# Kernel optimization log

Hardware: AMD Instinct MI355X
Metric: run time of the kernel (lower is better)

## Reference

```python
import jax, jax.numpy as jnp
import numpy as np

N_IN = 250000
N_OUT = 500000
INC = 256
OUTC = 128
KVOL = 8  # 2x2x2 transposed-conv kernel volume
BN_EPS = 1e-5


def setup_inputs() -> dict:
    key = jax.random.key(0)
    k1, k2, k3 = jax.random.split(key, 3)
    x = jax.random.normal(k1, (N_IN, INC), dtype=jnp.float32)
    # sparse conv weight: one [inc, outc] matrix per kernel offset
    W = jax.random.normal(k2, (KVOL, INC, OUTC), dtype=jnp.float32) * 0.02
    gamma = jnp.ones((OUTC,), dtype=jnp.float32)
    beta = jnp.zeros((OUTC,), dtype=jnp.float32)
    # kernel map: destination output voxel for each (kernel offset, input voxel)
    out_idx = jax.random.randint(k3, (KVOL, N_IN), 0, N_OUT, dtype=jnp.int32)
    return {"x": x, "W": W, "gamma": gamma, "beta": beta,
            "out_idx": out_idx, "n_out": N_OUT}


def reference(x, W, gamma, beta, out_idx, n_out):
    # --- sparse transposed conv3d: gather-matmul-scatter per kernel offset ---
    out = jnp.zeros((n_out, W.shape[-1]), dtype=x.dtype)
    for k in range(W.shape[0]):  # fixed small kernel volume (8)
        out = out.at[out_idx[k]].add(x @ W[k])
    # --- BatchNorm (training-mode batch stats over all output voxels) ---
    mean = jnp.mean(out, axis=0)
    var = jnp.mean(jnp.square(out - mean), axis=0)
    y = (out - mean) * jax.lax.rsqrt(var + BN_EPS) * gamma + beta
    return y
```

## Files before the change

### kernel.cpp

```cpp
#include <hip/hip_runtime.h>
#include <hip/hip_bf16.h>
#include <stdint.h>

#define N_IN 250000
#define N_OUT 500000
#define INC 256
#define OUTC 128
#define KVOL 8
#define NTOT (KVOL * N_IN)
#define BN_EPS 1e-5f

typedef __bf16 bf16x8_t __attribute__((ext_vector_type(8)));
typedef __bf16 bf16x4_t __attribute__((ext_vector_type(4)));
typedef float f32x4_t __attribute__((ext_vector_type(4)));

__device__ __forceinline__ __bf16 f2bf(float x) {
  union { float f; uint32_t u; } v; v.f = x;
  uint32_t r = v.u + 0x7FFFu + ((v.u >> 16) & 1u);
  uint16_t h = (uint16_t)(r >> 16);
  union { uint16_t s; __bf16 b; } o; o.s = h;
  return o.b;
}

__device__ __forceinline__ uint32_t pack2bf(float lo, float hi) {
  union { float f; uint32_t u; } a, b; a.f = lo; b.f = hi;
  uint32_t ra = a.u + 0x7FFFu + ((a.u >> 16) & 1u);
  uint32_t rb = b.u + 0x7FFFu + ((b.u >> 16) & 1u);
  return (ra >> 16) | (rb & 0xFFFF0000u);
}

__device__ __forceinline__ float bflo(uint32_t w) {
  union { uint32_t u; float f; } v; v.u = w << 16; return v.f;
}
__device__ __forceinline__ float bfhi(uint32_t w) {
  union { uint32_t u; float f; } v; v.u = w & 0xFFFF0000u; return v.f;
}

__global__ void wconv_kernel(const float* __restrict__ W, __bf16* __restrict__ Wt) {
  int f = blockIdx.x * blockDim.x + threadIdx.x;
  if (f >= KVOL * OUTC * INC) return;
  int i = f & (INC - 1);
  int o = (f >> 8) & (OUTC - 1);
  int k = f >> 15;
  Wt[f] = f2bf(W[(k * INC + i) * OUTC + o]);
}


__global__ void hist_kernel(const int* __restrict__ oidx, int* __restrict__ cnt) {
  int g = blockIdx.x * 256 + threadIdx.x;
  if (g < NTOT) atomicAdd(&cnt[oidx[g]], 1);
}

__global__ void scan1_kernel(const int* __restrict__ cnt, int* __restrict__ offs,
                             int* __restrict__ bsum) {
  __shared__ int sd[256];
  int t = threadIdx.x;
  int base = blockIdx.x * 1024 + t * 4;
  int v0 = 0, v1 = 0, v2 = 0, v3 = 0;
  if (base + 3 < N_OUT) {
    int4 v = *(const int4*)&cnt[base];
    v0 = v.x; v1 = v.y; v2 = v.z; v3 = v.w;
  } else {
    if (base     < N_OUT) v0 = cnt[base];
    if (base + 1 < N_OUT) v1 = cnt[base + 1];
    if (base + 2 < N_OUT) v2 = cnt[base + 2];
  }
  int s = v0 + v1 + v2 + v3;
  sd[t] = s; __syncthreads();
  for (int o = 1; o < 256; o <<= 1) {
    int a = (t >= o) ? sd[t - o] : 0;
    __syncthreads();
    sd[t] += a;
    __syncthreads();
  }
  int excl = sd[t] - s;
  if (base     < N_OUT) offs[base]     = excl;
  if (base + 1 < N_OUT) offs[base + 1] = excl + v0;
  if (base + 2 < N_OUT) offs[base + 2] = excl + v0 + v1;
  if (base + 3 < N_OUT) offs[base + 3] = excl + v0 + v1 + v2;
  if (t == 255) bsum[blockIdx.x] = sd[255];
}

__global__ void scan2_kernel(const int* __restrict__ bsum, int* __restrict__ bsumx, int nb) {
  __shared__ int sd[512];
  int t = threadIdx.x;
  int s = (t < nb) ? bsum[t] : 0;
  sd[t] = s; __syncthreads();
  for (int o = 1; o < 512; o <<= 1) {
    int a = (t >= o) ? sd[t - o] : 0;
    __syncthreads();
    sd[t] += a;
    __syncthreads();
  }
  if (t < nb) bsumx[t] = sd[t] - s;
}

__global__ void scan3_kernel(int* __restrict__ offs, int* __restrict__ cursor,
                             const int* __restrict__ bsumx) {
  int g = blockIdx.x * 256 + threadIdx.x;
  if (g < N_OUT) {
    int v = offs[g] + bsumx[g >> 10];
    offs[g] = v;
    cursor[g] = v;
  }
  if (g == 0) offs[N_OUT] = NTOT;
}

__global__ void fill_kernel(const int* __restrict__ oidx, int* __restrict__ cursor,
                            int* __restrict__ slot) {
  int g = blockIdx.x * 256 + threadIdx.x;
  if (g < NTOT) {
    int d = oidx[g];
    slot[g] = atomicAdd(&cursor[d], 1);
  }
}


#define TM 64
#define LDS_STRIDE 264

__global__ __launch_bounds__(512, 1) void gemm_store_kernel(
    const float* __restrict__ x, const __bf16* __restrict__ Wt,
    const int* __restrict__ slot, char* __restrict__ partials) {
  __shared__ __bf16 xs[TM * LDS_STRIDE];
  __shared__ uint2 stg[8][16][34];
  const int t = threadIdx.x;
  const int row0 = blockIdx.x * TM;

  #pragma unroll
  for (int i = 0; i < 8; ++i) {
    int f = t + i * 512;
    int r = f >> 6;
    int c4 = f & 63;
    int grow = row0 + r;
    float4 v = make_float4(0.f, 0.f, 0.f, 0.f);
    if (grow < N_IN) v = ((const float4*)x)[(size_t)grow * 64 + c4];
    bf16x4_t bv;
    bv[0] = f2bf(v.x); bv[1] = f2bf(v.y); bv[2] = f2bf(v.z); bv[3] = f2bf(v.w);
    *(bf16x4_t*)&xs[r * LDS_STRIDE + c4 * 4] = bv;
  }
  __syncthreads();

  const int w  = t >> 6;
  const int l  = t & 63;
  const int lr = l & 15;
  const int lg = l >> 4;

  f32x4_t accT[8][4];
  #pragma unroll
  for (int n = 0; n < 8; ++n)
    #pragma unroll
    for (int m = 0; m < 4; ++m)
      accT[n][m] = (f32x4_t){0.f, 0.f, 0.f, 0.f};

  const __bf16* Wk = Wt + (size_t)w * OUTC * INC;

  #pragma unroll
  for (int s = 0; s < 8; ++s) {
    bf16x8_t a[4], b[8];
    #pragma unroll
    for (int m = 0; m < 4; ++m)
      a[m] = *(const bf16x8_t*)&xs[(m * 16 + lr) * LDS_STRIDE + s * 32 + lg * 8];
    #pragma unroll
    for (int n = 0; n < 8; ++n)
      b[n] = *(const bf16x8_t*)&Wk[(n * 16 + lr) * INC + s * 32 + lg * 8];
    #pragma unroll
    for (int n = 0; n < 8; ++n)
      #pragma unroll
      for (int m = 0; m < 4; ++m)
        accT[n][m] = __builtin_amdgcn_mfma_f32_16x16x32_bf16(b[n], a[m], accT[n][m], 0, 0, 0);
  }

  const int r = l >> 2;
  const int p = l & 3;
  #pragma unroll
  for (int m = 0; m < 4; ++m) {
    #pragma unroll
    for (int n = 0; n < 8; ++n) {
      uint2 pk;
      pk.x = pack2bf(accT[n][m][0], accT[n][m][1]);
      pk.y = pack2bf(accT[n][m][2], accT[n][m][3]);
      stg[w][lr][n * 4 + lg] = pk;
    }
    __syncthreads();
    int grow = row0 + 16 * m + r;
    if (grow < N_IN) {
      int sl = slot[w * N_IN + grow];
      const uint4* rp = (const uint4*)&stg[w][r][0];
      char* dst = partials + (size_t)sl * 256 + p * 64;
      #pragma unroll
      for (int q = 0; q < 4; ++q)
        *(uint4*)(dst + q * 16) = rp[p * 4 + q];
    }
    __syncthreads();
  }
}


__global__ __launch_bounds__(256) void reduce_stats_kernel(
    const char* __restrict__ partials, const int* __restrict__ offs,
    char* __restrict__ accb, float* __restrict__ stats) {
  const int t = threadIdx.x;
  const int lane16 = t & 15;
  const int grp = t >> 4;
  float s[8], q[8];
  #pragma unroll
  for (int i = 0; i < 8; ++i) { s[i] = 0.f; q[i] = 0.f; }

  for (int d = blockIdx.x * 16 + grp; d < N_OUT; d += gridDim.x * 16) {
    int j0 = offs[d], j1 = offs[d + 1];
    float a[8];
    #pragma unroll
    for (int i = 0; i < 8; ++i) a[i] = 0.f;
    for (int j = j0; j < j1; ++j) {
      uint4 v = *(const uint4*)(partials + (size_t)j * 256 + lane16 * 16);
      a[0] += bflo(v.x); a[1] += bfhi(v.x);
      a[2] += bflo(v.y); a[3] += bfhi(v.y);
      a[4] += bflo(v.z); a[5] += bfhi(v.z);
      a[6] += bflo(v.w); a[7] += bfhi(v.w);
    }
    uint4 o;
    o.x = pack2bf(a[0], a[1]); o.y = pack2bf(a[2], a[3]);
    o.z = pack2bf(a[4], a[5]); o.w = pack2bf(a[6], a[7]);
    *(uint4*)(accb + (size_t)d * 512 + lane16 * 16) = o;
    uint32_t wd[4] = {o.x, o.y, o.z, o.w};
    #pragma unroll
    for (int u = 0; u < 4; ++u) {
      float f0 = bflo(wd[u]), f1 = bfhi(wd[u]);
      s[2 * u] += f0;     q[2 * u] += f0 * f0;
      s[2 * u + 1] += f1; q[2 * u + 1] += f1 * f1;
    }
  }

  __shared__ float reds[16][16][8];
  __shared__ float redq[16][16][8];
  #pragma unroll
  for (int i = 0; i < 8; ++i) { reds[grp][lane16][i] = s[i]; redq[grp][lane16][i] = q[i]; }
  __syncthreads();
  if (t < 128) {
    float acc = 0.f;
    #pragma unroll
    for (int g2 = 0; g2 < 16; ++g2) acc += reds[g2][t >> 3][t & 7];
    atomicAdd(&stats[t], acc);
  } else {
    int c = t - 128;
    float acc = 0.f;
    #pragma unroll
    for (int g2 = 0; g2 < 16; ++g2) acc += redq[g2][c >> 3][c & 7];
    atomicAdd(&stats[128 + c], acc);
  }
}

__global__ void norm_kernel(char* __restrict__ outb, const float* __restrict__ stats,
                            const float* __restrict__ gamma, const float* __restrict__ beta) {
  const int t = threadIdx.x;
  const int j = t & 15;
  const int ro = t >> 4;
  const float inv_n = 1.0f / (float)N_OUT;
  float sc[8], sh[8];
  #pragma unroll
  for (int i = 0; i < 8; ++i) {
    int c = j * 8 + i;
    float mean = stats[c] * inv_n;
    float var  = stats[128 + c] * inv_n - mean * mean;
    float s = gamma[c] * rsqrtf(var + BN_EPS);
    sc[i] = s;
    sh[i] = beta[c] - mean * s;
  }
  for (int r = blockIdx.x * 16 + ro; r < N_OUT; r += gridDim.x * 16) {
    uint4 v = *(const uint4*)(outb + (size_t)r * 512 + j * 16);
    uint32_t wds[4] = {v.x, v.y, v.z, v.w};
    f32x4_t o0, o1;
    #pragma unroll
    for (int u = 0; u < 4; ++u) {
      float f0 = bflo(wds[u]) * sc[2 * u] + sh[2 * u];
      float f1 = bfhi(wds[u]) * sc[2 * u + 1] + sh[2 * u + 1];
      if (u < 2) { o0[2 * u] = f0; o0[2 * u + 1] = f1; }
      else       { o1[2 * (u - 2)] = f0; o1[2 * (u - 2) + 1] = f1; }
    }
    *(f32x4_t*)(outb + (size_t)r * 512 + j * 32) = o0;
    *(f32x4_t*)(outb + (size_t)r * 512 + j * 32 + 16) = o1;
  }
}


__global__ __launch_bounds__(512, 1) void gemm_scatter_f32_kernel(
    const float* __restrict__ x, const __bf16* __restrict__ Wt,
    const int* __restrict__ out_idx, float* __restrict__ acc) {
  __shared__ __bf16 xs[TM * LDS_STRIDE];
  const int t = threadIdx.x;
  const int row0 = blockIdx.x * TM;
  #pragma unroll
  for (int i = 0; i < 8; ++i) {
    int f = t + i * 512;
    int r = f >> 6;
    int c4 = f & 63;
    int grow = row0 + r;
    float4 v = make_float4(0.f, 0.f, 0.f, 0.f);
    if (grow < N_IN) v = ((const float4*)x)[(size_t)grow * 64 + c4];
    bf16x4_t bv;
    bv[0] = f2bf(v.x); bv[1] = f2bf(v.y); bv[2] = f2bf(v.z); bv[3] = f2bf(v.w);
    *(bf16x4_t*)&xs[r * LDS_STRIDE + c4 * 4] = bv;
  }
  __syncthreads();
  const int w = t >> 6, l = t & 63, lr = l & 15, lg = l >> 4;
  f32x4_t accr[4][8];
  #pragma unroll
  for (int m = 0; m < 4; ++m)
    #pragma unroll
    for (int n = 0; n < 8; ++n)
      accr[m][n] = (f32x4_t){0.f, 0.f, 0.f, 0.f};
  const __bf16* Wk = Wt + (size_t)w * OUTC * INC;
  #pragma unroll
  for (int s = 0; s < 8; ++s) {
    bf16x8_t a[4], b[8];
    #pragma unroll
    for (int m = 0; m < 4; ++m)
      a[m] = *(const bf16x8_t*)&xs[(m * 16 + lr) * LDS_STRIDE + s * 32 + lg * 8];
    #pragma unroll
    for (int n = 0; n < 8; ++n)
      b[n] = *(const bf16x8_t*)&Wk[(n * 16 + lr) * INC + s * 32 + lg * 8];
    #pragma unroll
    for (int m = 0; m < 4; ++m)
      #pragma unroll
      for (int n = 0; n < 8; ++n)
        accr[m][n] = __builtin_amdgcn_mfma_f32_16x16x32_bf16(a[m], b[n], accr[m][n], 0, 0, 0);
  }
  const int* oidx = out_idx + (size_t)w * N_IN;
  #pragma unroll
  for (int m = 0; m < 4; ++m) {
    int rbase = m * 16 + lg * 4;
    #pragma unroll
    for (int reg = 0; reg < 4; ++reg) {
      int grow = row0 + rbase + reg;
      if (grow < N_IN) {
        int dst = oidx[grow];
        float* ap = acc + (size_t)dst * OUTC;
        #pragma unroll
        for (int n = 0; n < 8; ++n)
          atomicAdd(&ap[n * 16 + lr], accr[m][n][reg]);
      }
    }
  }
}

__global__ void stats_f32_kernel(const float* __restrict__ acc, float* __restrict__ stats) {
  const int t = threadIdx.x;
  const int c4 = t & 31;
  const int ro = t >> 5;
  f32x4_t s = {0.f, 0.f, 0.f, 0.f}, q = {0.f, 0.f, 0.f, 0.f};
  for (int r = blockIdx.x * 8 + ro; r < N_OUT; r += gridDim.x * 8) {
    f32x4_t v = ((const f32x4_t*)acc)[(size_t)r * 32 + c4];
    s += v; q += v * v;
  }
  __shared__ float red[256][8];
  #pragma unroll
  for (int j = 0; j < 4; ++j) { red[t][j] = s[j]; red[t][4 + j] = q[j]; }
  __syncthreads();
  if (t < 32) {
    float S[4] = {0.f, 0.f, 0.f, 0.f}, Q[4] = {0.f, 0.f, 0.f, 0.f};
    for (int r2 = 0; r2 < 8; ++r2)
      #pragma unroll
      for (int j = 0; j < 4; ++j) {
        S[j] += red[r2 * 32 + t][j];
        Q[j] += red[r2 * 32 + t][4 + j];
      }
    #pragma unroll
    for (int j = 0; j < 4; ++j) {
      atomicAdd(&stats[t * 4 + j], S[j]);
      atomicAdd(&stats[128 + t * 4 + j], Q[j]);
    }
  }
}

__global__ void norm_f32_kernel(float* __restrict__ out, const float* __restrict__ stats,
                                const float* __restrict__ gamma, const float* __restrict__ beta) {
  const int t = threadIdx.x;
  const int c4 = t & 31;
  const int ro = t >> 5;
  const float inv_n = 1.0f / (float)N_OUT;
  float sc[4], sh[4];
  #pragma unroll
  for (int j = 0; j < 4; ++j) {
    int c = c4 * 4 + j;
    float mean = stats[c] * inv_n;
    float var  = stats[128 + c] * inv_n - mean * mean;
    float s = gamma[c] * rsqrtf(var + BN_EPS);
    sc[j] = s;
    sh[j] = beta[c] - mean * s;
  }
  for (int r = blockIdx.x * 8 + ro; r < N_OUT; r += gridDim.x * 8) {
    f32x4_t v = ((const f32x4_t*)out)[(size_t)r * 32 + c4];
    #pragma unroll
    for (int j = 0; j < 4; ++j) v[j] = v[j] * sc[j] + sh[j];
    ((f32x4_t*)out)[(size_t)r * 32 + c4] = v;
  }
}


extern "C" void kernel_launch(void* const* d_in, const int* in_sizes, int n_in,
                              void* d_out, int out_size, void* d_ws, size_t ws_size,
                              hipStream_t stream) {
  const float* x     = (const float*)d_in[0];
  const float* W     = (const float*)d_in[1];
  const float* gamma = (const float*)d_in[2];
  const float* beta  = (const float*)d_in[3];
  const int*   oidx  = (const int*)d_in[4];

  const size_t P_OFF     = 0;
  const size_t SLOT_OFF  = 512000000;
  const size_t CNT_OFF   = 520000000;
  const size_t OFFS_OFF  = 522000000;
  const size_t CURS_OFF  = 524000384;
  const size_t BSUM_OFF  = 526000384;
  const size_t BSUMX_OFF = 526004480;
  const size_t WT_OFF    = 526008576;
  const size_t STATS_OFF = 526532864;
  const size_t NEED      = 526533888;

  if (ws_size >= NEED) {
    char* ws = (char*)d_ws;
    char* partials = ws + P_OFF;
    int* slot   = (int*)(ws + SLOT_OFF);
    int* cnt    = (int*)(ws + CNT_OFF);
    int* offs   = (int*)(ws + OFFS_OFF);
    int* cursor = (int*)(ws + CURS_OFF);
    int* bsum   = (int*)(ws + BSUM_OFF);
    int* bsumx  = (int*)(ws + BSUMX_OFF);
    __bf16* Wt  = (__bf16*)(ws + WT_OFF);
    float* stats = (float*)(ws + STATS_OFF);

    hipMemsetAsync(cnt, 0, N_OUT * sizeof(int), stream);
    hipMemsetAsync(stats, 0, 256 * sizeof(float), stream);

    wconv_kernel<<<(KVOL * OUTC * INC + 255) / 256, 256, 0, stream>>>(W, Wt);
    hist_kernel<<<(NTOT + 255) / 256, 256, 0, stream>>>(oidx, cnt);
    const int NB1 = (N_OUT + 1023) / 1024;
    scan1_kernel<<<NB1, 256, 0, stream>>>(cnt, offs, bsum);
    scan2_kernel<<<1, 512, 0, stream>>>(bsum, bsumx, NB1);
    scan3_kernel<<<(N_OUT + 255) / 256, 256, 0, stream>>>(offs, cursor, bsumx);
    fill_kernel<<<(NTOT + 255) / 256, 256, 0, stream>>>(oidx, cursor, slot);
    gemm_store_kernel<<<(N_IN + TM - 1) / TM, 512, 0, stream>>>(x, Wt, slot, partials);
    reduce_stats_kernel<<<2048, 256, 0, stream>>>(partials, offs, (char*)d_out, stats);
    norm_kernel<<<512, 256, 0, stream>>>((char*)d_out, stats, gamma, beta);
  } else {
    __bf16* Wt   = (__bf16*)d_ws;
    float* stats = (float*)((char*)d_ws + (size_t)KVOL * OUTC * INC * 2);
    float* out = (float*)d_out;

    hipMemsetAsync(d_out, 0, (size_t)N_OUT * OUTC * sizeof(float), stream);
    hipMemsetAsync(stats, 0, 256 * sizeof(float), stream);

    wconv_kernel<<<(KVOL * OUTC * INC + 255) / 256, 256, 0, stream>>>(W, Wt);
    gemm_scatter_f32_kernel<<<(N_IN + TM - 1) / TM, 512, 0, stream>>>(x, Wt, oidx, out);
    stats_f32_kernel<<<1024, 256, 0, stream>>>(out, stats);
    norm_f32_kernel<<<2048, 256, 0, stream>>>(out, stats, gamma, beta);
  }
}
```

Baseline: 918.0 us.

## Sort inputs per kernel offset and gather rows so partial writes are localized

Builds per-offset destination-sorted orderings of input rows via extra histogram/scan/fill passes, pre-converts x to bf16 once, and launches the GEMM per (row tile, offset) gathering x rows in sorted order. The intent is to make partial-sum stores land in nearby slots instead of scattered ones, improving write locality. It adds extra atomics, scan kernels and gather reads, reduces per-block weight reuse, and uses the output buffer as scratch space.

```diff
diff --git a/kernel.cpp b/kernel.cpp
--- a/kernel.cpp
+++ b/kernel.cpp
@@ -9,6 +9,7 @@
 #define KVOL 8
 #define NTOT (KVOL * N_IN)
 #define BN_EPS 1e-5f
+#define DCHUNKS 489
 
 typedef __bf16 bf16x8_t __attribute__((ext_vector_type(8)));
 typedef __bf16 bf16x4_t __attribute__((ext_vector_type(4)));
@@ -17,8 +18,7 @@
 __device__ __forceinline__ __bf16 f2bf(float x) {
   union { float f; uint32_t u; } v; v.f = x;
   uint32_t r = v.u + 0x7FFFu + ((v.u >> 16) & 1u);
-  uint16_t h = (uint16_t)(r >> 16);
-  union { uint16_t s; __bf16 b; } o; o.s = h;
+  union { uint16_t s; __bf16 b; } o; o.s = (uint16_t)(r >> 16);
   return o.b;
 }
 
@@ -34,6 +34,18 @@
 }
 __device__ __forceinline__ float bfhi(uint32_t w) {
   union { uint32_t u; float f; } v; v.u = w & 0xFFFF0000u; return v.f;
+}
+
+
+__global__ void xconv_kernel(const float* __restrict__ x, uint32_t* __restrict__ xb) {
+  int g = blockIdx.x * 256 + threadIdx.x;
+  if (g >= N_IN * INC / 8) return;
+  const float4* p = (const float4*)x + (size_t)g * 2;
+  float4 v0 = p[0], v1 = p[1];
+  uint4 o;
+  o.x = pack2bf(v0.x, v0.y); o.y = pack2bf(v0.z, v0.w);
+  o.z = pack2bf(v1.x, v1.y); o.w = pack2bf(v1.z, v1.w);
+  ((uint4*)xb)[g] = o;
 }
 
 __global__ void wconv_kernel(const float* __restrict__ W, __bf16* __restrict__ Wt) {
@@ -46,87 +58,264 @@
 }
 
 
-__global__ void hist_kernel(const int* __restrict__ oidx, int* __restrict__ cnt) {
-  int g = blockIdx.x * 256 + threadIdx.x;
-  if (g < NTOT) atomicAdd(&cnt[oidx[g]], 1);
-}
-
-__global__ void scan1_kernel(const int* __restrict__ cnt, int* __restrict__ offs,
-                             int* __restrict__ bsum) {
+__global__ void hist8_kernel(const int* __restrict__ oidx, int* __restrict__ cnt8,
+                             int* __restrict__ gcnt) {
+  int i = blockIdx.x * 256 + threadIdx.x;
+  int k = blockIdx.y;
+  if (i < N_IN) {
+    int d = oidx[k * N_IN + i];
+    atomicAdd(&cnt8[k * N_OUT + d], 1);
+    atomicAdd(&gcnt[d], 1);
+  }
+}
+
+__global__ void scan1s_kernel(const int* __restrict__ in, int* __restrict__ out,
+                              int* __restrict__ bsum) {
   __shared__ int sd[256];
   int t = threadIdx.x;
+  int s = blockIdx.y;
+  const int* inp = in + (size_t)s * N_OUT;
+  int* outp = out + (size_t)s * N_OUT;
   int base = blockIdx.x * 1024 + t * 4;
   int v0 = 0, v1 = 0, v2 = 0, v3 = 0;
   if (base + 3 < N_OUT) {
-    int4 v = *(const int4*)&cnt[base];
+    int4 v = *(const int4*)&inp[base];
     v0 = v.x; v1 = v.y; v2 = v.z; v3 = v.w;
   } else {
-    if (base     < N_OUT) v0 = cnt[base];
-    if (base + 1 < N_OUT) v1 = cnt[base + 1];
-    if (base + 2 < N_OUT) v2 = cnt[base + 2];
-  }
-  int s = v0 + v1 + v2 + v3;
-  sd[t] = s; __syncthreads();
+    if (base     < N_OUT) v0 = inp[base];
+    if (base + 1 < N_OUT) v1 = inp[base + 1];
+    if (base + 2 < N_OUT) v2 = inp[base + 2];
+  }
+  int sm = v0 + v1 + v2 + v3;
+  sd[t] = sm; __syncthreads();
   for (int o = 1; o < 256; o <<= 1) {
     int a = (t >= o) ? sd[t - o] : 0;
     __syncthreads();
     sd[t] += a;
     __syncthreads();
   }
-  int excl = sd[t] - s;
-  if (base     < N_OUT) offs[base]     = excl;
-  if (base + 1 < N_OUT) offs[base + 1] = excl + v0;
-  if (base + 2 < N_OUT) offs[base + 2] = excl + v0 + v1;
-  if (base + 3 < N_OUT) offs[base + 3] = excl + v0 + v1 + v2;
-  if (t == 255) bsum[blockIdx.x] = sd[255];
-}
-
-__global__ void scan2_kernel(const int* __restrict__ bsum, int* __restrict__ bsumx, int nb) {
+  int excl = sd[t] - sm;
+  if (base     < N_OUT) outp[base]     = excl;
+  if (base + 1 < N_OUT) outp[base + 1] = excl + v0;
+  if (base + 2 < N_OUT) outp[base + 2] = excl + v0 + v1;
+  if (base + 3 < N_OUT) outp[base + 3] = excl + v0 + v1 + v2;
+  if (t == 255) bsum[s * DCHUNKS + blockIdx.x] = sd[255];
+}
+
+__global__ void scan2s_kernel(const int* __restrict__ bsum, int* __restrict__ bsumx) {
   __shared__ int sd[512];
   int t = threadIdx.x;
-  int s = (t < nb) ? bsum[t] : 0;
-  sd[t] = s; __syncthreads();
+  int s = blockIdx.x;
+  int v = (t < DCHUNKS) ? bsum[s * DCHUNKS + t] : 0;
+  sd[t] = v; __syncthreads();
   for (int o = 1; o < 512; o <<= 1) {
     int a = (t >= o) ? sd[t - o] : 0;
     __syncthreads();
     sd[t] += a;
     __syncthreads();
   }
-  if (t < nb) bsumx[t] = sd[t] - s;
-}
-
-__global__ void scan3_kernel(int* __restrict__ offs, int* __restrict__ cursor,
-                             const int* __restrict__ bsumx) {
+  if (t < DCHUNKS) bsumx[s * DCHUNKS + t] = sd[t] - v;
+}
+
+__global__ void scan3s_kernel(int* __restrict__ cur8, const int* __restrict__ bsumx) {
+  int g = blockIdx.x * 256 + threadIdx.x;
+  int s = blockIdx.y;
+  if (g < N_OUT) cur8[(size_t)s * N_OUT + g] += bsumx[s * DCHUNKS + (g >> 10)];
+}
+
+__global__ void scan3g_kernel(int* __restrict__ goffs, int* __restrict__ gcur,
+                              const int* __restrict__ bsumx) {
   int g = blockIdx.x * 256 + threadIdx.x;
   if (g < N_OUT) {
-    int v = offs[g] + bsumx[g >> 10];
-    offs[g] = v;
-    cursor[g] = v;
-  }
-  if (g == 0) offs[N_OUT] = NTOT;
-}
-
-__global__ void fill_kernel(const int* __restrict__ oidx, int* __restrict__ cursor,
-                            int* __restrict__ slot) {
-  int g = blockIdx.x * 256 + threadIdx.x;
-  if (g < NTOT) {
-    int d = oidx[g];
-    slot[g] = atomicAdd(&cursor[d], 1);
-  }
-}
-
-
-#define TM 64
+    int v = goffs[g] + bsumx[g >> 10];
+    goffs[g] = v;
+    gcur[g] = v;
+  }
+  if (g == 0) goffs[N_OUT] = NTOT;
+}
+
+__global__ void fill_kernel(const int* __restrict__ oidx, int* __restrict__ cur8,
+                            int* __restrict__ gcur, int* __restrict__ ssrc,
+                            int* __restrict__ sgslot) {
+  int i = blockIdx.x * 256 + threadIdx.x;
+  int k = blockIdx.y;
+  if (i < N_IN) {
+    int d = oidx[k * N_IN + i];
+    int j = atomicAdd(&cur8[(size_t)k * N_OUT + d], 1);
+    int g = atomicAdd(&gcur[d], 1);
+    ssrc[k * N_IN + j] = i;
+    sgslot[k * N_IN + j] = g;
+  }
+}
+
+
+#define GTM 64
 #define LDS_STRIDE 264
 
-__global__ __launch_bounds__(512, 1) void gemm_store_kernel(
+__global__ __launch_bounds__(512, 1) void gemm_gather_store_kernel(
+    const uint32_t* __restrict__ xb, const __bf16* __restrict__ Wt,
+    const int* __restrict__ ssrc, const int* __restrict__ sgslot,
+    char* __restrict__ partials) {
+  __shared__ __bf16 xs[GTM * LDS_STRIDE];
+  __shared__ uint2 stg[GTM][34];
+  __shared__ int s_src[GTM], s_gsl[GTM];
+  const int t = threadIdx.x;
+  const int k = blockIdx.y;
+  const int slot0 = blockIdx.x * GTM;
+
+  if (t < GTM) {
+    int sl = slot0 + t;
+    s_src[t] = (sl < N_IN) ? ssrc[k * N_IN + sl] : -1;
+    s_gsl[t] = (sl < N_IN) ? sgslot[k * N_IN + sl] : -1;
+  }
+  __syncthreads();
+
+  #pragma unroll
+  for (int ii = 0; ii < 4; ++ii) {
+    int r = ii * 16 + (t >> 5);
+    int off = t & 31;
+    int src = s_src[r];
+    uint4 v = {0u, 0u, 0u, 0u};
+    if (src >= 0) v = *(const uint4*)((const char*)xb + (size_t)src * 512 + off * 16);
+    *(uint4*)&xs[r * LDS_STRIDE + off * 8] = v;
+  }
+  __syncthreads();
+
+  const int w = t >> 6, l = t & 63, lr = l & 15, lg = l >> 4;
+  const int m  = w >> 1;
+  const int nh = w & 1;
+
+  f32x4_t accT[4];
+  #pragma unroll
+  for (int n = 0; n < 4; ++n) accT[n] = (f32x4_t){0.f, 0.f, 0.f, 0.f};
+
+  const __bf16* Wk = Wt + (size_t)k * OUTC * INC;
+
+  #pragma unroll
+  for (int s = 0; s < 8; ++s) {
+    bf16x8_t a = *(const bf16x8_t*)&xs[(m * 16 + lr) * LDS_STRIDE + s * 32 + lg * 8];
+    #pragma unroll
+    for (int n = 0; n < 4; ++n) {
+      bf16x8_t b = *(const bf16x8_t*)&Wk[((nh * 4 + n) * 16 + lr) * INC + s * 32 + lg * 8];
+      accT[n] = __builtin_amdgcn_mfma_f32_16x16x32_bf16(b, a, accT[n], 0, 0, 0);
+    }
+  }
+
+  #pragma unroll
+  for (int n = 0; n < 4; ++n) {
+    uint2 pk;
+    pk.x = pack2bf(accT[n][0], accT[n][1]);
+    pk.y = pack2bf(accT[n][2], accT[n][3]);
+    stg[m * 16 + lr][(nh * 4 + n) * 4 + lg] = pk;
+  }
+  __syncthreads();
+
+  {
+    int r = t >> 3, p = t & 7;
+    int gs = s_gsl[r];
+    if (gs >= 0) {
+      const uint4* rp = (const uint4*)&stg[r][0];
+      char* dst = partials + (size_t)gs * 256 + p * 32;
+      *(uint4*)(dst)      = rp[p * 2];
+      *(uint4*)(dst + 16) = rp[p * 2 + 1];
+    }
+  }
+}
+
+
+__global__ __launch_bounds__(256) void reduce_stats_kernel(
+    const char* __restrict__ partials, const int* __restrict__ goffs,
+    char* __restrict__ accb, float* __restrict__ stats) {
+  const int t = threadIdx.x;
+  const int lane16 = t & 15;
+  const int grp = t >> 4;
+  float s[8], q[8];
+  #pragma unroll
+  for (int i = 0; i < 8; ++i) { s[i] = 0.f; q[i] = 0.f; }
+
+  for (int d = blockIdx.x * 16 + grp; d < N_OUT; d += gridDim.x * 16) {
+    int j0 = goffs[d], j1 = goffs[d + 1];
+    float a[8];
+    #pragma unroll
+    for (int i = 0; i < 8; ++i) a[i] = 0.f;
+    for (int j = j0; j < j1; ++j) {
+      uint4 v = *(const uint4*)(partials + (size_t)j * 256 + lane16 * 16);
+      a[0] += bflo(v.x); a[1] += bfhi(v.x);
+      a[2] += bflo(v.y); a[3] += bfhi(v.y);
+      a[4] += bflo(v.z); a[5] += bfhi(v.z);
+      a[6] += bflo(v.w); a[7] += bfhi(v.w);
+    }
+    uint4 o;
+    o.x = pack2bf(a[0], a[1]); o.y = pack2bf(a[2], a[3]);
+    o.z = pack2bf(a[4], a[5]); o.w = pack2bf(a[6], a[7]);
+    *(uint4*)(accb + (size_t)d * 512 + lane16 * 16) = o;
+    uint32_t wd[4] = {o.x, o.y, o.z, o.w};
+    #pragma unroll
+    for (int u = 0; u < 4; ++u) {
+      float f0 = bflo(wd[u]), f1 = bfhi(wd[u]);
+      s[2 * u] += f0;     q[2 * u] += f0 * f0;
+      s[2 * u + 1] += f1; q[2 * u + 1] += f1 * f1;
+    }
+  }
+
+  __shared__ float reds[16][16][8];
+  __shared__ float redq[16][16][8];
+  #pragma unroll
+  for (int i = 0; i < 8; ++i) { reds[grp][lane16][i] = s[i]; redq[grp][lane16][i] = q[i]; }
+  __syncthreads();
+  if (t < 128) {
+    float acc = 0.f;
+    #pragma unroll
+    for (int g2 = 0; g2 < 16; ++g2) acc += reds[g2][t >> 3][t & 7];
+    atomicAdd(&stats[t], acc);
+  } else {
+    int c = t - 128;
+    float acc = 0.f;
+    #pragma unroll
+    for (int g2 = 0; g2 < 16; ++g2) acc += redq[g2][c >> 3][c & 7];
+    atomicAdd(&stats[128 + c], acc);
+  }
+}
+
+__global__ void norm_kernel(char* __restrict__ outb, const float* __restrict__ stats,
+                            const float* __restrict__ gamma, const float* __restrict__ beta) {
+  const int t = threadIdx.x;
+  const int j = t & 15;
+  const int ro = t >> 4;
+  const float inv_n = 1.0f / (float)N_OUT;
+  float sc[8], sh[8];
+  #pragma unroll
+  for (int i = 0; i < 8; ++i) {
+    int c = j * 8 + i;
+    float mean = stats[c] * inv_n;
+    float var  = stats[128 + c] * inv_n - mean * mean;
+    float s = gamma[c] * rsqrtf(var + BN_EPS);
+    sc[i] = s;
+    sh[i] = beta[c] - mean * s;
+  }
+  for (int r = blockIdx.x * 16 + ro; r < N_OUT; r += gridDim.x * 16) {
+    uint4 v = *(const uint4*)(outb + (size_t)r * 512 + j * 16);
+    uint32_t wds[4] = {v.x, v.y, v.z, v.w};
+    f32x4_t o0, o1;
+    #pragma unroll
+    for (int u = 0; u < 4; ++u) {
+      float f0 = bflo(wds[u]) * sc[2 * u] + sh[2 * u];
+      float f1 = bfhi(wds[u]) * sc[2 * u + 1] + sh[2 * u + 1];
+      if (u < 2) { o0[2 * u] = f0; o0[2 * u + 1] = f1; }
+      else       { o1[2 * (u - 2)] = f0; o1[2 * (u - 2) + 1] = f1; }
+    }
+    *(f32x4_t*)(outb + (size_t)r * 512 + j * 32) = o0;
+    *(f32x4_t*)(outb + (size_t)r * 512 + j * 32 + 16) = o1;
+  }
+}
+
+
+__global__ __launch_bounds__(512, 1) void gemm_scatter_f32_kernel(
     const float* __restrict__ x, const __bf16* __restrict__ Wt,
-    const int* __restrict__ slot, char* __restrict__ partials) {
-  __shared__ __bf16 xs[TM * LDS_STRIDE];
-  __shared__ uint2 stg[8][16][34];
-  const int t = threadIdx.x;
-  const int row0 = blockIdx.x * TM;
-
+    const int* __restrict__ out_idx, float* __restrict__ acc) {
+  __shared__ __bf16 xs[GTM * LDS_STRIDE];
+  const int t = threadIdx.x;
+  const int row0 = blockIdx.x * GTM;
   #pragma unroll
   for (int i = 0; i < 8; ++i) {
     int f = t + i * 512;
@@ -140,169 +329,6 @@
     *(bf16x4_t*)&xs[r * LDS_STRIDE + c4 * 4] = bv;
   }
   __syncthreads();
-
-  const int w  = t >> 6;
-  const int l  = t & 63;
-  const int lr = l & 15;
-  const int lg = l >> 4;
-
-  f32x4_t accT[8][4];
-  #pragma unroll
-  for (int n = 0; n < 8; ++n)
-    #pragma unroll
-    for (int m = 0; m < 4; ++m)
-      accT[n][m] = (f32x4_t){0.f, 0.f, 0.f, 0.f};
-
-  const __bf16* Wk = Wt + (size_t)w * OUTC * INC;
-
-  #pragma unroll
-  for (int s = 0; s < 8; ++s) {
-    bf16x8_t a[4], b[8];
-    #pragma unroll
-    for (int m = 0; m < 4; ++m)
-      a[m] = *(const bf16x8_t*)&xs[(m * 16 + lr) * LDS_STRIDE + s * 32 + lg * 8];
-    #pragma unroll
-    for (int n = 0; n < 8; ++n)
-      b[n] = *(const bf16x8_t*)&Wk[(n * 16 + lr) * INC + s * 32 + lg * 8];
-    #pragma unroll
-    for (int n = 0; n < 8; ++n)
-      #pragma unroll
-      for (int m = 0; m < 4; ++m)
-        accT[n][m] = __builtin_amdgcn_mfma_f32_16x16x32_bf16(b[n], a[m], accT[n][m], 0, 0, 0);
-  }
-
-  const int r = l >> 2;
-  const int p = l & 3;
-  #pragma unroll
-  for (int m = 0; m < 4; ++m) {
-    #pragma unroll
-    for (int n = 0; n < 8; ++n) {
-      uint2 pk;
-      pk.x = pack2bf(accT[n][m][0], accT[n][m][1]);
-      pk.y = pack2bf(accT[n][m][2], accT[n][m][3]);
-      stg[w][lr][n * 4 + lg] = pk;
-    }
-    __syncthreads();
-    int grow = row0 + 16 * m + r;
-    if (grow < N_IN) {
-      int sl = slot[w * N_IN + grow];
-      const uint4* rp = (const uint4*)&stg[w][r][0];
-      char* dst = partials + (size_t)sl * 256 + p * 64;
-      #pragma unroll
-      for (int q = 0; q < 4; ++q)
-        *(uint4*)(dst + q * 16) = rp[p * 4 + q];
-    }
-    __syncthreads();
-  }
-}
-
-
-__global__ __launch_bounds__(256) void reduce_stats_kernel(
-    const char* __restrict__ partials, const int* __restrict__ offs,
-    char* __restrict__ accb, float* __restrict__ stats) {
-  const int t = threadIdx.x;
-  const int lane16 = t & 15;
-  const int grp = t >> 4;
-  float s[8], q[8];
-  #pragma unroll
-  for (int i = 0; i < 8; ++i) { s[i] = 0.f; q[i] = 0.f; }
-
-  for (int d = blockIdx.x * 16 + grp; d < N_OUT; d += gridDim.x * 16) {
-    int j0 = offs[d], j1 = offs[d + 1];
-    float a[8];
-    #pragma unroll
-    for (int i = 0; i < 8; ++i) a[i] = 0.f;
-    for (int j = j0; j < j1; ++j) {
-      uint4 v = *(const uint4*)(partials + (size_t)j * 256 + lane16 * 16);
-      a[0] += bflo(v.x); a[1] += bfhi(v.x);
-      a[2] += bflo(v.y); a[3] += bfhi(v.y);
-      a[4] += bflo(v.z); a[5] += bfhi(v.z);
-      a[6] += bflo(v.w); a[7] += bfhi(v.w);
-    }
-    uint4 o;
-    o.x = pack2bf(a[0], a[1]); o.y = pack2bf(a[2], a[3]);
-    o.z = pack2bf(a[4], a[5]); o.w = pack2bf(a[6], a[7]);
-    *(uint4*)(accb + (size_t)d * 512 + lane16 * 16) = o;
-    uint32_t wd[4] = {o.x, o.y, o.z, o.w};
-    #pragma unroll
-    for (int u = 0; u < 4; ++u) {
-      float f0 = bflo(wd[u]), f1 = bfhi(wd[u]);
-      s[2 * u] += f0;     q[2 * u] += f0 * f0;
-      s[2 * u + 1] += f1; q[2 * u + 1] += f1 * f1;
-    }
-  }
-
-  __shared__ float reds[16][16][8];
-  __shared__ float redq[16][16][8];
-  #pragma unroll
-  for (int i = 0; i < 8; ++i) { reds[grp][lane16][i] = s[i]; redq[grp][lane16][i] = q[i]; }
-  __syncthreads();
-  if (t < 128) {
-    float acc = 0.f;
-    #pragma unroll
-    for (int g2 = 0; g2 < 16; ++g2) acc += reds[g2][t >> 3][t & 7];
-    atomicAdd(&stats[t], acc);
-  } else {
-    int c = t - 128;
-    float acc = 0.f;
-    #pragma unroll
-    for (int g2 = 0; g2 < 16; ++g2) acc += redq[g2][c >> 3][c & 7];
-    atomicAdd(&stats[128 + c], acc);
-  }
-}
-
-__global__ void norm_kernel(char* __restrict__ outb, const float* __restrict__ stats,
-                            const float* __restrict__ gamma, const float* __restrict__ beta) {
-  const int t = threadIdx.x;
-  const int j = t & 15;
-  const int ro = t >> 4;
-  const float inv_n = 1.0f / (float)N_OUT;
-  float sc[8], sh[8];
-  #pragma unroll
-  for (int i = 0; i < 8; ++i) {
-    int c = j * 8 + i;
-    float mean = stats[c] * inv_n;
-    float var  = stats[128 + c] * inv_n - mean * mean;
-    float s = gamma[c] * rsqrtf(var + BN_EPS);
-    sc[i] = s;
-    sh[i] = beta[c] - mean * s;
-  }
-  for (int r = blockIdx.x * 16 + ro; r < N_OUT; r += gridDim.x * 16) {
-    uint4 v = *(const uint4*)(outb + (size_t)r * 512 + j * 16);
-    uint32_t wds[4] = {v.x, v.y, v.z, v.w};
-    f32x4_t o0, o1;
-    #pragma unroll
-    for (int u = 0; u < 4; ++u) {
-      float f0 = bflo(wds[u]) * sc[2 * u] + sh[2 * u];
-      float f1 = bfhi(wds[u]) * sc[2 * u + 1] + sh[2 * u + 1];
-      if (u < 2) { o0[2 * u] = f0; o0[2 * u + 1] = f1; }
-      else       { o1[2 * (u - 2)] = f0; o1[2 * (u - 2) + 1] = f1; }
-    }
-    *(f32x4_t*)(outb + (size_t)r * 512 + j * 32) = o0;
-    *(f32x4_t*)(outb + (size_t)r * 512 + j * 32 + 16) = o1;
-  }
-}
-
-
-__global__ __launch_bounds__(512, 1) void gemm_scatter_f32_kernel(
-    const float* __restrict__ x, const __bf16* __restrict__ Wt,
-    const int* __restrict__ out_idx, float* __restrict__ acc) {
-  __shared__ __bf16 xs[TM * LDS_STRIDE];
-  const int t = threadIdx.x;
-  const int row0 = blockIdx.x * TM;
-  #pragma unroll
-  for (int i = 0; i < 8; ++i) {
-    int f = t + i * 512;
-    int r = f >> 6;
-    int c4 = f & 63;
-    int grow = row0 + r;
-    float4 v = make_float4(0.f, 0.f, 0.f, 0.f);
-    if (grow < N_IN) v = ((const float4*)x)[(size_t)grow * 64 + c4];
-    bf16x4_t bv;
-    bv[0] = f2bf(v.x); bv[1] = f2bf(v.y); bv[2] = f2bf(v.z); bv[3] = f2bf(v.w);
-    *(bf16x4_t*)&xs[r * LDS_STRIDE + c4 * 4] = bv;
-  }
-  __syncthreads();
   const int w = t >> 6, l = t & 63, lr = l & 15, lg = l >> 4;
   f32x4_t accr[4][8];
   #pragma unroll
@@ -407,42 +433,50 @@
   const float* beta  = (const float*)d_in[3];
   const int*   oidx  = (const int*)d_in[4];
 
-  const size_t P_OFF     = 0;
-  const size_t SLOT_OFF  = 512000000;
-  const size_t CNT_OFF   = 520000000;
-  const size_t OFFS_OFF  = 522000000;
-  const size_t CURS_OFF  = 524000384;
-  const size_t BSUM_OFF  = 526000384;
-  const size_t BSUMX_OFF = 526004480;
-  const size_t WT_OFF    = 526008576;
-  const size_t STATS_OFF = 526532864;
-  const size_t NEED      = 526533888;
+  const size_t PART_OFF  = 0;
+  const size_t GOFFS_OFF = 512000000;
+  const size_t STATS_OFF = 514000016;
+  const size_t NEED      = 514001040;
 
   if (ws_size >= NEED) {
     char* ws = (char*)d_ws;
-    char* partials = ws + P_OFF;
-    int* slot   = (int*)(ws + SLOT_OFF);
-    int* cnt    = (int*)(ws + CNT_OFF);
-    int* offs   = (int*)(ws + OFFS_OFF);
-    int* cursor = (int*)(ws + CURS_OFF);
-    int* bsum   = (int*)(ws + BSUM_OFF);
-    int* bsumx  = (int*)(ws + BSUMX_OFF);
-    __bf16* Wt  = (__bf16*)(ws + WT_OFF);
+    char* partials = ws + PART_OFF;
+    int* goffs  = (int*)(ws + GOFFS_OFF);
     float* stats = (float*)(ws + STATS_OFF);
 
-    hipMemsetAsync(cnt, 0, N_OUT * sizeof(int), stream);
+    char* ob = (char*)d_out;
+    uint32_t* xb   = (uint32_t*)(ob);
+    int* cnt8      = (int*)(ob + 128000000);
+    int* cur8      = (int*)(ob + 144000000);
+    int* gcnt      = (int*)(ob + 160000000);
+    int* gcur      = (int*)(ob + 162000000);
+    int* ssrc      = (int*)(ob + 164000016);
+    int* sgslot    = (int*)(ob + 172000016);
+    __bf16* Wt     = (__bf16*)(ob + 180000016);
+    int* bsum8     = (int*)(ob + 180524304);
+    int* bsumx8    = (int*)(ob + 180539952);
+    int* gbsum     = (int*)(ob + 180555600);
+    int* gbsumx    = (int*)(ob + 180557568);
+
+    hipMemsetAsync(cnt8, 0, (size_t)KVOL * N_OUT * sizeof(int), stream);
+    hipMemsetAsync(gcnt, 0, (size_t)N_OUT * sizeof(int), stream);
     hipMemsetAsync(stats, 0, 256 * sizeof(float), stream);
 
+    xconv_kernel<<<(N_IN * INC / 8 + 255) / 256, 256, 0, stream>>>(x, xb);
     wconv_kernel<<<(KVOL * OUTC * INC + 255) / 256, 256, 0, stream>>>(W, Wt);
-    hist_kernel<<<(NTOT + 255) / 256, 256, 0, stream>>>(oidx, cnt);
-    const int NB1 = (N_OUT + 1023) / 1024;
-    scan1_kernel<<<NB1, 256, 0, stream>>>(cnt, offs, bsum);
-    scan2_kernel<<<1, 512, 0, stream>>>(bsum, bsumx, NB1);
-    scan3_kernel<<<(N_OUT + 255) / 256, 256, 0, stream>>>(offs, cursor, bsumx);
-    fill_kernel<<<(NTOT + 255) / 256, 256, 0, stream>>>(oidx, cursor, slot);
-    gemm_store_kernel<<<(N_IN + TM - 1) / TM, 512, 0, stream>>>(x, Wt, slot, partials);
-    reduce_stats_kernel<<<2048, 256, 0, stream>>>(partials, offs, (char*)d_out, stats);
-    norm_kernel<<<512, 256, 0, stream>>>((char*)d_out, stats, gamma, beta);
+    hist8_kernel<<<dim3((N_IN + 255) / 256, KVOL), 256, 0, stream>>>(oidx, cnt8, gcnt);
+    scan1s_kernel<<<dim3(DCHUNKS, KVOL), 256, 0, stream>>>(cnt8, cur8, bsum8);
+    scan2s_kernel<<<KVOL, 512, 0, stream>>>(bsum8, bsumx8);
+    scan3s_kernel<<<dim3((N_OUT + 255) / 256, KVOL), 256, 0, stream>>>(cur8, bsumx8);
+    scan1s_kernel<<<dim3(DCHUNKS, 1), 256, 0, stream>>>(gcnt, goffs, gbsum);
+    scan2s_kernel<<<1, 512, 0, stream>>>(gbsum, gbsumx);
+    scan3g_kernel<<<(N_OUT + 255) / 256, 256, 0, stream>>>(goffs, gcur, gbsumx);
+    fill_kernel<<<dim3((N_IN + 255) / 256, KVOL), 256, 0, stream>>>(
+        oidx, cur8, gcur, ssrc, sgslot);
+    gemm_gather_store_kernel<<<dim3((N_IN + GTM - 1) / GTM, KVOL), 512, 0, stream>>>(
+        xb, Wt, ssrc, sgslot, partials);
+    reduce_stats_kernel<<<2048, 256, 0, stream>>>(partials, goffs, ob, stats);
+    norm_kernel<<<1024, 256, 0, stream>>>(ob, stats, gamma, beta);
   } else {
     __bf16* Wt   = (__bf16*)d_ws;
     float* stats = (float*)((char*)d_ws + (size_t)KVOL * OUTC * INC * 2);
@@ -452,7 +486,7 @@
     hipMemsetAsync(stats, 0, 256 * sizeof(float), stream);
 
     wconv_kernel<<<(KVOL * OUTC * INC + 255) / 256, 256, 0, stream>>>(W, Wt);
-    gemm_scatter_f32_kernel<<<(N_IN + TM - 1) / TM, 512, 0, stream>>>(x, Wt, oidx, out);
+    gemm_scatter_f32_kernel<<<(N_IN + GTM - 1) / GTM, 512, 0, stream>>>(x, Wt, oidx, out);
     stats_f32_kernel<<<1024, 256, 0, stream>>>(out, stats);
     norm_f32_kernel<<<2048, 256, 0, stream>>>(out, stats, gamma, beta);
   }
```

After: 1.813 ms. +97.5%, slower.
